# Kernel optimization log

Measured on AMD Instinct MI355X. Metric: run time of the kernel, lower is better.

The kernel has to match this reference:

```python
import jax, jax.numpy as jnp
import numpy as np

EMBED_DIM = 1024
NUM_HEADS = 16
HEAD_DIM = EMBED_DIM // NUM_HEADS
B, T = 4, 2048


def quantum_layer(x):
    # Exact closed form of the RY + CNOT-chain + PauliZ circuit:
    # expval(Z_i) = prod_{j<=i} cos(x_j)  (cumulative product along feature dim)
    return jnp.cumprod(jnp.cos(x), axis=-1)


def separate_heads(x):
    b, s, _ = x.shape
    return x.reshape(b, s, NUM_HEADS, HEAD_DIM).transpose(0, 2, 1, 3)  # (B,H,T,D)


def combine_heads(x):
    b, h, s, d = x.shape
    return x.transpose(0, 2, 1, 3).reshape(b, s, h * d)


def setup_inputs() -> dict:
    key = jax.random.key(0)
    ks = jax.random.split(key, 9)
    scale = 1.0 / np.sqrt(EMBED_DIM)
    return {
        "x": jax.random.normal(ks[0], (B, T, EMBED_DIM), dtype=jnp.float32),
        "Wq": jax.random.normal(ks[1], (EMBED_DIM, EMBED_DIM), dtype=jnp.float32) * scale,
        "bq": jax.random.normal(ks[2], (EMBED_DIM,), dtype=jnp.float32) * 0.01,
        "Wk": jax.random.normal(ks[3], (EMBED_DIM, EMBED_DIM), dtype=jnp.float32) * scale,
        "bk": jax.random.normal(ks[4], (EMBED_DIM,), dtype=jnp.float32) * 0.01,
        "Wv": jax.random.normal(ks[5], (EMBED_DIM, EMBED_DIM), dtype=jnp.float32) * scale,
        "bv": jax.random.normal(ks[6], (EMBED_DIM,), dtype=jnp.float32) * 0.01,
        "Wo": jax.random.normal(ks[7], (EMBED_DIM, EMBED_DIM), dtype=jnp.float32) * scale,
        "bo": jax.random.normal(ks[8], (EMBED_DIM,), dtype=jnp.float32) * 0.01,
    }


def reference(x, Wq, bq, Wk, bk, Wv, bv, Wo, bo):
    k = x @ Wk + bk
    q = x @ Wq + bq
    v = x @ Wv + bv
    # quantum circuit applied to q and k projections
    q = quantum_layer(q)
    k = quantum_layer(k)
    # NOTE: source swaps roles: kqv = (heads(k), heads(q), heads(v)); q, h, v = kqv
    qh = separate_heads(k)   # acts as query
    kh = separate_heads(q)   # acts as key
    vh = separate_heads(v)
    scores = jnp.einsum("bhqd,bhkd->bhqk", qh, kh) / jnp.sqrt(jnp.float32(HEAD_DIM))
    attn = jax.nn.softmax(scores, axis=-1)  # dropout is identity in eval
    out = jnp.einsum("bhqk,bhkd->bhqd", attn, vh)
    return combine_heads(out) @ Wo + bo
```

## Files before the change

### kernel.cpp

```cpp
#include <hip/hip_runtime.h>
#include <hip/hip_bf16.h>
#include <stdint.h>

#define B_ 4
#define T_ 2048
#define E_ 1024
#define H_ 16
#define D_ 64
#define M_ (B_ * T_)

typedef unsigned short u16;
typedef unsigned int u32;
typedef short s16x8 __attribute__((ext_vector_type(8)));
typedef unsigned short u16x8 __attribute__((ext_vector_type(8)));
typedef float f32x4 __attribute__((ext_vector_type(4)));
typedef unsigned int u32x2 __attribute__((ext_vector_type(2)));

#define LP_ 72

__device__ __forceinline__ u16 f2bf(float f) {
    __hip_bfloat16 h = __float2bfloat16(f);
    return __builtin_bit_cast(u16, h);
}
__device__ __forceinline__ float bf2f(u16 u) {
    unsigned int v = ((unsigned int)u) << 16;
    return __builtin_bit_cast(float, v);
}
__device__ __forceinline__ u32 pk2(float a, float b) {
    return (u32)f2bf(a) | ((u32)f2bf(b) << 16);
}

__device__ __forceinline__ int block_probe_is_bf16(const void* x, int tid) {
    const u16* p = (const u16*)x;
    u16 u = p[tid];
    int e = (u >> 7) & 0xFF;
    int ok = ((u & 0x7FFF) == 0 || (e >= 103 && e <= 133)) ? 1 : 0;
    return (__syncthreads_count(ok) >= 240) ? 1 : 0;
}

__device__ __forceinline__ void load_a_regs(
    int a_bf, const u16* abase_bf, const float* abase_f, int kk, u16x8 (&av)[4])
{
    if (a_bf) {
        #pragma unroll
        for (int j = 0; j < 4; j++) av[j] = *(const u16x8*)(abase_bf + kk + j * 8);
    } else {
        #pragma unroll
        for (int j = 0; j < 4; j++) {
            f32x4 t0 = *(const f32x4*)(abase_f + kk + j * 8);
            f32x4 t1 = *(const f32x4*)(abase_f + kk + j * 8 + 4);
            u16x8 o;
            #pragma unroll
            for (int e = 0; e < 4; e++) { o[e] = f2bf(t0[e]); o[4 + e] = f2bf(t1[e]); }
            av[j] = o;
        }
    }
}
__device__ __forceinline__ void load_b_regs(const u16* bbase, int kk, u16x8 (&bv)[4]) {
    #pragma unroll
    for (int j = 0; j < 4; j++) bv[j] = *(const u16x8*)(bbase + kk + j * 8);
}
__device__ __forceinline__ void write_lds72(
    u16* l, int srow, int soff, const u16x8 (&v)[4])
{
    #pragma unroll
    for (int j = 0; j < 4; j++)
        *(u16x8*)&l[srow * LP_ + soff + j * 8] = v[j];
}
__device__ __forceinline__ void mfma_tile72(
    const u16* al, const u16* bl, f32x4 (&acc)[4][4],
    int wm, int wn, int lane15, int quad)
{
    #pragma unroll
    for (int ks = 0; ks < 2; ks++) {
        s16x8 af[4], bfr[4];
        #pragma unroll
        for (int i = 0; i < 4; i++)
            af[i] = *(const s16x8*)&al[(wm + i * 16 + lane15) * LP_ + ks * 32 + quad * 8];
        #pragma unroll
        for (int j = 0; j < 4; j++)
            bfr[j] = *(const s16x8*)&bl[(wn + j * 16 + lane15) * LP_ + ks * 32 + quad * 8];
        #pragma unroll
        for (int i = 0; i < 4; i++)
            #pragma unroll
            for (int j = 0; j < 4; j++)
                acc[i][j] = __builtin_amdgcn_mfma_f32_16x16x32_bf16(af[i], bfr[j], acc[i][j], 0, 0, 0);
    }
}

__global__ __launch_bounds__(256) void transpose_w4_kernel(
    const void* __restrict__ w0, const void* __restrict__ w1,
    const void* __restrict__ w2, const void* __restrict__ w3,
    u16* __restrict__ o0, u16* __restrict__ o1,
    u16* __restrict__ o2, u16* __restrict__ o3,
    const void* __restrict__ xprobe)
{
    __shared__ u16 th[64][66];
    const int x = threadIdx.x, y = threadIdx.y;
    const int isbf = block_probe_is_bf16(xprobe, y * 64 + x);
    const int z = (int)blockIdx.z;
    const void* in = (z == 0) ? w0 : (z == 1) ? w1 : (z == 2) ? w2 : w3;
    u16* o = (z == 0) ? o0 : (z == 1) ? o1 : (z == 2) ? o2 : o3;
    const int r0 = blockIdx.y * 64;
    const int c0 = blockIdx.x * 64;
    #pragma unroll
    for (int j = 0; j < 16; j++) {
        const size_t idx = (size_t)(r0 + y * 16 + j) * E_ + c0 + x;
        float v = isbf ? bf2f(((const u16*)in)[idx]) : ((const float*)in)[idx];
        th[y * 16 + j][x] = f2bf(v);
    }
    __syncthreads();
    #pragma unroll
    for (int j = 0; j < 16; j++)
        o[(size_t)(c0 + y * 16 + j) * E_ + r0 + x] = th[x][y * 16 + j];
}

__global__ __launch_bounds__(256) void convert_bias_kernel(
    const void* __restrict__ bq, const void* __restrict__ bk,
    const void* __restrict__ bv, const void* __restrict__ bo,
    float* __restrict__ outb, const void* __restrict__ xprobe)
{
    const int isbf = block_probe_is_bf16(xprobe, threadIdx.x);
    const int i = blockIdx.x * 256 + threadIdx.x;
    const int w = blockIdx.y;
    const void* p = (w == 0) ? bq : (w == 1) ? bk : (w == 2) ? bv : bo;
    float v = isbf ? bf2f(((const u16*)p)[i]) : ((const float*)p)[i];
    outb[w * 1024 + i] = v;
}

__global__ __launch_bounds__(256) void gemm_f32out_kernel(
    const void* __restrict__ A, int a_mode, int m_base,
    const u16* __restrict__ Bt, const float* __restrict__ bias,
    float* __restrict__ Cout, int ldc)
{
    __shared__ u16 a_lds[128 * LP_];
    __shared__ u16 b_lds[128 * LP_];
    const int tid = threadIdx.x;
    const int isbf = block_probe_is_bf16(A, tid);
    const int a_bf = (a_mode < 0) ? isbf : a_mode;
    const int wave = tid >> 6, lane = tid & 63;
    const int lane15 = lane & 15, quad = lane >> 4;
    const int wm = (wave & 1) * 64, wn = (wave >> 1) * 64;
    const int nwg = (int)(gridDim.x * gridDim.y);
    const int lin = (int)(blockIdx.y * gridDim.x + blockIdx.x);
    const int swz = (lin & 7) * (nwg >> 3) + (lin >> 3);
    const int m0 = (swz / (int)gridDim.x) * 128;
    const int n0 = (swz % (int)gridDim.x) * 128;
    const int srow = tid >> 1;
    const int soff = (tid & 1) * 32;

    f32x4 acc[4][4];
    #pragma unroll
    for (int i = 0; i < 4; i++)
        #pragma unroll
        for (int j = 0; j < 4; j++) acc[i][j] = (f32x4)0.0f;

    const u16* abase_bf = (const u16*)A + (size_t)(m_base + m0 + srow) * E_ + soff;
    const float* abase_f = (const float*)A + (size_t)(m_base + m0 + srow) * E_ + soff;
    const u16* bbase = Bt + (size_t)(n0 + srow) * E_ + soff;

    u16x8 av[4], bv[4];
    load_a_regs(a_bf, abase_bf, abase_f, 0, av);
    load_b_regs(bbase, 0, bv);

    for (int kk = 0; kk < E_; kk += 64) {
        __syncthreads();
        write_lds72(a_lds, srow, soff, av);
        write_lds72(b_lds, srow, soff, bv);
        __syncthreads();
        if (kk + 64 < E_) {
            load_a_regs(a_bf, abase_bf, abase_f, kk + 64, av);
            load_b_regs(bbase, kk + 64, bv);
        }
        mfma_tile72(a_lds, b_lds, acc, wm, wn, lane15, quad);
    }

    #pragma unroll
    for (int j = 0; j < 4; j++) {
        const int col = n0 + wn + j * 16 + lane15;
        const float bb = bias[col];
        #pragma unroll
        for (int i = 0; i < 4; i++) {
            const int row = m0 + wm + i * 16 + quad * 4;
            #pragma unroll
            for (int r = 0; r < 4; r++)
                Cout[(size_t)(row + r) * ldc + col] = acc[i][j][r] + bb;
        }
    }
}

__global__ __launch_bounds__(256) void gemm_qkv_kernel(
    const void* __restrict__ A, const u16* __restrict__ Bt,
    const float* __restrict__ bias, float* __restrict__ Cout,
    u16* __restrict__ Vt)
{
    __shared__ u16 smem[2 * 128 * LP_];
    u16* a_lds = smem;
    u16* b_lds = smem + 128 * LP_;
    const int tid = threadIdx.x;
    const int isbf = block_probe_is_bf16(A, tid);
    const int wave = tid >> 6, lane = tid & 63;
    const int lane15 = lane & 15, quad = lane >> 4;
    const int wm = (wave & 1) * 64, wn = (wave >> 1) * 64;
    const int nwg = (int)(gridDim.x * gridDim.y);
    const int lin = (int)(blockIdx.y * gridDim.x + blockIdx.x);
    const int swz = (lin & 7) * (nwg >> 3) + (lin >> 3);
    const int m0 = (swz / (int)gridDim.x) * 128;
    const int n0 = (swz % (int)gridDim.x) * 128;
    const int srow = tid >> 1;
    const int soff = (tid & 1) * 32;

    f32x4 acc[4][4];
    #pragma unroll
    for (int i = 0; i < 4; i++)
        #pragma unroll
        for (int j = 0; j < 4; j++) acc[i][j] = (f32x4)0.0f;

    const u16* abase_bf = (const u16*)A + (size_t)(m0 + srow) * E_ + soff;
    const float* abase_f = (const float*)A + (size_t)(m0 + srow) * E_ + soff;
    const u16* bbase = Bt + (size_t)(n0 + srow) * E_ + soff;

    u16x8 av[4], bv[4];
    load_a_regs(isbf, abase_bf, abase_f, 0, av);
    load_b_regs(bbase, 0, bv);

    for (int kk = 0; kk < E_; kk += 64) {
        __syncthreads();
        write_lds72(a_lds, srow, soff, av);
        write_lds72(b_lds, srow, soff, bv);
        __syncthreads();
        if (kk + 64 < E_) {
            load_a_regs(isbf, abase_bf, abase_f, kk + 64, av);
            load_b_regs(bbase, kk + 64, bv);
        }
        mfma_tile72(a_lds, b_lds, acc, wm, wn, lane15, quad);
    }

    if (n0 < 2048) {
        #pragma unroll
        for (int j = 0; j < 4; j++) {
            const int col = n0 + wn + j * 16 + lane15;
            const float bb = bias[col];
            #pragma unroll
            for (int i = 0; i < 4; i++) {
                const int row = m0 + wm + i * 16 + quad * 4;
                #pragma unroll
                for (int r = 0; r < 4; r++)
                    Cout[(size_t)(row + r) * 2048 + col] = acc[i][j][r] + bb;
            }
        }
    } else {
        __syncthreads();
        u16* c_tile = smem;
        #pragma unroll
        for (int j = 0; j < 4; j++) {
            const float bb = bias[n0 + wn + j * 16 + lane15];
            #pragma unroll
            for (int i = 0; i < 4; i++)
                #pragma unroll
                for (int r = 0; r < 4; r++)
                    c_tile[(wm + i * 16 + quad * 4 + r) * 132 + wn + j * 16 + lane15] =
                        f2bf(acc[i][j][r] + bb);
        }
        __syncthreads();
        const int b = m0 >> 11, t0 = m0 & 2047;
        const int orow = tid >> 1, half = tid & 1;
        const int n0v = n0 - 2048;
        u16* dst = Vt + ((size_t)b * 1024 + n0v + orow) * T_ + t0 + half * 64;
        #pragma unroll
        for (int c = 0; c < 8; c++) {
            u16x8 o;
            #pragma unroll
            for (int e = 0; e < 8; e++)
                o[e] = c_tile[(half * 64 + c * 8 + e) * 132 + orow];
            *(u16x8*)(dst + c * 8) = o;
        }
    }
}

__global__ __launch_bounds__(256) void gemm_v_fused_kernel(
    const void* __restrict__ X, const u16* __restrict__ Bt,
    const float* __restrict__ bias, u16* __restrict__ Vt)
{
    __shared__ u16 smem[2 * 128 * 72];
    u16* a_lds = smem;
    u16* b_lds = smem + 128 * 72;
    const int tid = threadIdx.x;
    const int isbf = block_probe_is_bf16(X, tid);
    const int wave = tid >> 6, lane = tid & 63;
    const int lane15 = lane & 15, quad = lane >> 4;
    const int wm = (wave & 1) * 64, wn = (wave >> 1) * 64;
    const int nwg = (int)(gridDim.x * gridDim.y);
    const int lin = (int)(blockIdx.y * gridDim.x + blockIdx.x);
    const int swz = (lin & 7) * (nwg >> 3) + (lin >> 3);
    const int m0 = (swz / (int)gridDim.x) * 128;
    const int n0 = (swz % (int)gridDim.x) * 128;
    const int srow = tid >> 1;
    const int soff = (tid & 1) * 32;

    f32x4 acc[4][4];
    #pragma unroll
    for (int i = 0; i < 4; i++)
        #pragma unroll
        for (int j = 0; j < 4; j++) acc[i][j] = (f32x4)0.0f;

    const u16* abase_bf = (const u16*)X + (size_t)(m0 + srow) * E_ + soff;
    const float* abase_f = (const float*)X + (size_t)(m0 + srow) * E_ + soff;
    const u16* bbase = Bt + (size_t)(n0 + srow) * E_ + soff;

    u16x8 av[4], bv[4];
    load_a_regs(isbf, abase_bf, abase_f, 0, av);
    load_b_regs(bbase, 0, bv);

    for (int kk = 0; kk < E_; kk += 64) {
        __syncthreads();
        #pragma unroll
        for (int j = 0; j < 4; j++) {
            *(u16x8*)&a_lds[srow * 72 + soff + j * 8] = av[j];
            *(u16x8*)&b_lds[srow * 72 + soff + j * 8] = bv[j];
        }
        __syncthreads();
        if (kk + 64 < E_) {
            load_a_regs(isbf, abase_bf, abase_f, kk + 64, av);
            load_b_regs(bbase, kk + 64, bv);
        }
        #pragma unroll
        for (int ks = 0; ks < 2; ks++) {
            s16x8 af[4], bfr[4];
            #pragma unroll
            for (int i = 0; i < 4; i++)
                af[i] = *(const s16x8*)&a_lds[(wm + i * 16 + lane15) * 72 + ks * 32 + quad * 8];
            #pragma unroll
            for (int j = 0; j < 4; j++)
                bfr[j] = *(const s16x8*)&b_lds[(wn + j * 16 + lane15) * 72 + ks * 32 + quad * 8];
            #pragma unroll
            for (int i = 0; i < 4; i++)
                #pragma unroll
                for (int j = 0; j < 4; j++)
                    acc[i][j] = __builtin_amdgcn_mfma_f32_16x16x32_bf16(af[i], bfr[j], acc[i][j], 0, 0, 0);
        }
    }

    __syncthreads();
    u16* c_tile = smem;
    #pragma unroll
    for (int j = 0; j < 4; j++) {
        const float bb = bias[n0 + wn + j * 16 + lane15];
        #pragma unroll
        for (int i = 0; i < 4; i++)
            #pragma unroll
            for (int r = 0; r < 4; r++)
                c_tile[(wm + i * 16 + quad * 4 + r) * 132 + wn + j * 16 + lane15] =
                    f2bf(acc[i][j][r] + bb);
    }
    __syncthreads();
    const int b = m0 >> 11, t0 = m0 & 2047;
    const int orow = tid >> 1, half = tid & 1;
    u16* dst = Vt + ((size_t)b * 1024 + n0 + orow) * T_ + t0 + half * 64;
    #pragma unroll
    for (int c = 0; c < 8; c++) {
        u16x8 o;
        #pragma unroll
        for (int e = 0; e < 8; e++)
            o[e] = c_tile[(half * 64 + c * 8 + e) * 132 + orow];
        *(u16x8*)(dst + c * 8) = o;
    }
}

__global__ __launch_bounds__(256) void quantum2_kernel(
    const float* __restrict__ in, u16* __restrict__ key, u16* __restrict__ qry)
{
    const int wave = threadIdx.x >> 6, lane = threadIdx.x & 63;
    const int unit = (int)blockIdx.x * 4 + wave;
    const int row = unit >> 1, seg = unit & 1;
    const float* p = in + (size_t)row * 2048 + seg * 1024 + lane * 16;
    float v[16];
    #pragma unroll
    for (int j = 0; j < 16; j += 4) {
        f32x4 t = *(const f32x4*)(p + j);
        v[j] = t[0]; v[j + 1] = t[1]; v[j + 2] = t[2]; v[j + 3] = t[3];
    }
    float pl[16];
    float run = 1.0f;
    #pragma unroll
    for (int j = 0; j < 16; j++) { run *= cosf(v[j]); pl[j] = run; }
    float incl = run;
    #pragma unroll
    for (int off = 1; off < 64; off <<= 1) {
        float t = __shfl_up(incl, off);
        if (lane >= off) incl *= t;
    }
    float pref = __shfl_up(incl, 1);
    if (lane == 0) pref = 1.0f;
    u16x8 o0, o1;
    #pragma unroll
    for (int j = 0; j < 8; j++) {
        o0[j] = f2bf(pref * pl[j]);
        o1[j] = f2bf(pref * pl[j + 8]);
    }
    u16* outp = (seg ? qry : key) + (size_t)row * E_ + lane * 16;
    *(u16x8*)(outp) = o0;
    *(u16x8*)(outp + 8) = o1;
}

__global__ __launch_bounds__(256) void attn_kernel(
    const u16* __restrict__ Qrm, const u16* __restrict__ Krm,
    const u16* __restrict__ Vt, u16* __restrict__ Orm)
{
    __shared__ u16 k_lds[64 * 72];
    __shared__ u16 v_lds[64 * 72];
    __shared__ u16 p_lds[128 * 72];
    const int tid = threadIdx.x;
    const int wave = tid >> 6, lane = tid & 63;
    const int lane15 = lane & 15, quad = lane >> 4;

    const int lin = (int)(blockIdx.x + gridDim.x * blockIdx.y);
    const int swz = (lin & 7) * 128 + (lin >> 3);
    const int t0 = (swz & 15) * 128;
    const int bh = swz >> 4;
    const int b = bh >> 4, h = bh & 15;

    s16x8 qf[2][2];
    #pragma unroll
    for (int mt = 0; mt < 2; mt++)
        #pragma unroll
        for (int ks = 0; ks < 2; ks++) {
            const u16* src = Qrm
                + (size_t)(b * T_ + t0 + wave * 32 + mt * 16 + lane15) * E_
                + h * 64 + ks * 32 + quad * 8;
            u16x8 t = *(const u16x8*)src;
            u16x8 o;
            #pragma unroll
            for (int e = 0; e < 8; e++) o[e] = f2bf(bf2f(t[e]) * 0.125f);
            qf[mt][ks] = __builtin_bit_cast(s16x8, o);
        }

    f32x4 lsum4[2];
    f32x4 oacc[2][4];
    #pragma unroll
    for (int mt = 0; mt < 2; mt++) {
        lsum4[mt] = (f32x4)0.0f;
        #pragma unroll
        for (int n = 0; n < 4; n++) oacc[mt][n] = (f32x4)0.0f;
    }

    const u16* kbase = Krm + (size_t)(b * T_) * E_ + h * 64;
    const u16* vbase = Vt + (size_t)bh * 64 * T_;
    const int srow = tid >> 2;
    const int soff = (tid & 3) * 16;

    u16x8 kpre0, kpre1, vpre0, vpre1;
    {
        const u16* ksrc = kbase + (size_t)srow * E_ + soff;
        kpre0 = *(const u16x8*)(ksrc);
        kpre1 = *(const u16x8*)(ksrc + 8);
        const u16* vsrc = vbase + (size_t)srow * T_ + soff;
        vpre0 = *(const u16x8*)(vsrc);
        vpre1 = *(const u16x8*)(vsrc + 8);
    }

    for (int tk0 = 0; tk0 < T_; tk0 += 64) {
        __syncthreads();
        *(u16x8*)&k_lds[srow * 72 + soff]     = kpre0;
        *(u16x8*)&k_lds[srow * 72 + soff + 8] = kpre1;
        *(u16x8*)&v_lds[srow * 72 + soff]     = vpre0;
        *(u16x8*)&v_lds[srow * 72 + soff + 8] = vpre1;
        __syncthreads();

        if (tk0 + 64 < T_) {
            const u16* ksrc = kbase + (size_t)(tk0 + 64 + srow) * E_ + soff;
            kpre0 = *(const u16x8*)(ksrc);
            kpre1 = *(const u16x8*)(ksrc + 8);
            const u16* vsrc = vbase + (size_t)srow * T_ + tk0 + 64 + soff;
            vpre0 = *(const u16x8*)(vsrc);
            vpre1 = *(const u16x8*)(vsrc + 8);
        }

        f32x4 sacc[2][4];
        #pragma unroll
        for (int mt = 0; mt < 2; mt++)
            #pragma unroll
            for (int j = 0; j < 4; j++) sacc[mt][j] = (f32x4)0.0f;
        #pragma unroll
        for (int ks = 0; ks < 2; ks++) {
            s16x8 kb[4];
            #pragma unroll
            for (int j = 0; j < 4; j++)
                kb[j] = *(const s16x8*)&k_lds[(j * 16 + lane15) * 72 + ks * 32 + quad * 8];
            #pragma unroll
            for (int mt = 0; mt < 2; mt++)
                #pragma unroll
                for (int j = 0; j < 4; j++)
                    sacc[mt][j] = __builtin_amdgcn_mfma_f32_16x16x32_bf16(
                        kb[j], qf[mt][ks], sacc[mt][j], 0, 0, 0);
        }

        #pragma unroll
        for (int mt = 0; mt < 2; mt++)
            #pragma unroll
            for (int j = 0; j < 4; j++) {
                const f32x4 s = sacc[mt][j];
                const float p0 = __expf(s[0]);
                const float p1 = __expf(s[1]);
                const float p2 = __expf(s[2]);
                const float p3 = __expf(s[3]);
                lsum4[mt][0] += p0; lsum4[mt][1] += p1;
                lsum4[mt][2] += p2; lsum4[mt][3] += p3;
                u32x2 w;
                w[0] = pk2(p0, p1);
                w[1] = pk2(p2, p3);
                *(u32x2*)&p_lds[(wave * 32 + mt * 16 + lane15) * 72 + j * 16 + quad * 4] = w;
            }

        #pragma unroll
        for (int ks = 0; ks < 2; ks++) {
            s16x8 pa[2], vb[4];
            #pragma unroll
            for (int mt = 0; mt < 2; mt++)
                pa[mt] = *(const s16x8*)&p_lds[(wave * 32 + mt * 16 + lane15) * 72 + ks * 32 + quad * 8];
            #pragma unroll
            for (int n = 0; n < 4; n++)
                vb[n] = *(const s16x8*)&v_lds[(n * 16 + lane15) * 72 + ks * 32 + quad * 8];
            #pragma unroll
            for (int mt = 0; mt < 2; mt++)
                #pragma unroll
                for (int n = 0; n < 4; n++)
                    oacc[mt][n] = __builtin_amdgcn_mfma_f32_16x16x32_bf16(
                        pa[mt], vb[n], oacc[mt][n], 0, 0, 0);
        }
    }

    #pragma unroll
    for (int mt = 0; mt < 2; mt++) {
        float l = lsum4[mt][0] + lsum4[mt][1] + lsum4[mt][2] + lsum4[mt][3];
        l += __shfl_xor(l, 16);
        l += __shfl_xor(l, 32);
        #pragma unroll
        for (int r = 0; r < 4; r++) {
            const float lr = __shfl(l, quad * 4 + r);
            const float inv = 1.0f / lr;
            const size_t row = (size_t)(b * T_ + t0 + wave * 32 + mt * 16 + quad * 4 + r);
            #pragma unroll
            for (int n = 0; n < 4; n++)
                Orm[row * E_ + h * 64 + n * 16 + lane15] = f2bf(oacc[mt][n][r] * inv);
        }
    }
}

extern "C" void kernel_launch(void* const* d_in, const int* in_sizes, int n_in,
                              void* d_out, int out_size, void* d_ws, size_t ws_size,
                              hipStream_t stream) {
    (void)in_sizes; (void)n_in; (void)out_size;
    const void* x  = d_in[0];
    const void* Wq = d_in[1];
    const void* bq = d_in[2];
    const void* Wk = d_in[3];
    const void* bk = d_in[4];
    const void* Wv = d_in[5];
    const void* bv = d_in[6];
    const void* Wo = d_in[7];
    const void* bo = d_in[8];

    char* ws = (char*)d_ws;
    const size_t MB = 1024 * 1024;
    u16*   wt_o   = (u16*)(ws);
    float* biasf  = (float*)(ws + 2 * MB);
    u16*   wt_qkv = (u16*)(ws + 3 * MB);
    u16*   key    = (u16*)(ws + 9 * MB);
    u16*   qry    = (u16*)(ws + 25 * MB);

    transpose_w4_kernel<<<dim3(16, 16, 4), dim3(64, 4), 0, stream>>>(
        Wq, Wk, Wv, Wo,
        wt_qkv, wt_qkv + 1024 * 1024, wt_qkv + 2 * 1024 * 1024, wt_o, x);
    convert_bias_kernel<<<dim3(4, 4), 256, 0, stream>>>(
        bq, bk, bv, bo, biasf, x);

    if (ws_size >= (size_t)121 * MB) {
        u16*   vt  = (u16*)(ws + 41 * MB);
        float* tmp = (float*)(ws + 57 * MB);
        u16*   orm = (u16*)(ws + 57 * MB);
        gemm_qkv_kernel<<<dim3(24, 64), 256, 0, stream>>>(
            x, wt_qkv, biasf, tmp, vt);
        quantum2_kernel<<<4096, 256, 0, stream>>>(tmp, key, qry);
        attn_kernel<<<dim3(16, 64), 256, 0, stream>>>(qry, key, vt, orm);
        gemm_f32out_kernel<<<dim3(8, 64), 256, 0, stream>>>(
            orm, 1, 0, wt_o, biasf + 3 * 1024, (float*)d_out, 1024);
    } else {
        float* tmp = (float*)(ws + 41 * MB);
        u16*   vt  = (u16*)(ws + 41 * MB);
        u16*   orm = (u16*)(ws + 57 * MB);
        for (int hh = 0; hh < 2; hh++) {
            gemm_f32out_kernel<<<dim3(16, 32), 256, 0, stream>>>(
                x, -1, hh * 4096, wt_qkv, biasf, tmp, 2048);
            quantum2_kernel<<<2048, 256, 0, stream>>>(
                tmp, key + (size_t)hh * 4096 * E_, qry + (size_t)hh * 4096 * E_);
        }
        gemm_v_fused_kernel<<<dim3(8, 64), 256, 0, stream>>>(
            x, wt_qkv + 2 * 1024 * 1024, biasf + 2 * 1024, vt);
        attn_kernel<<<dim3(16, 64), 256, 0, stream>>>(qry, key, vt, orm);
        gemm_f32out_kernel<<<dim3(8, 64), 256, 0, stream>>>(
            orm, 1, 0, wt_o, biasf + 3 * 1024, (float*)d_out, 1024);
    }
}
```

Baseline: 376.2 us.

## Stage QKV GEMM tiles via global_load_lds with double-buffered LDS pipeline

Rewrites the QKV projection GEMM main loop to copy bf16 A and B tiles directly from global memory into LDS using the global_load_lds builtin. The tiles are double-buffered so the next K-slice loads while MFMAs run on the current one, with explicit vmcnt waits and raw barriers. This removes the register round-trip and the separate LDS writes. In exchange LDS use doubles, the unpadded 64-wide layout may cause bank conflicts, and the fp32 fallback path still converts through registers. The MFMA section is also wrapped in s_setprio.

Measured after the change: 410.6 us. +9.2%, slower.

```diff
diff --git a/kernel.cpp b/kernel.cpp
--- a/kernel.cpp
+++ b/kernel.cpp
@@ -30,6 +30,15 @@
     return (u32)f2bf(a) | ((u32)f2bf(b) << 16);
 }
 
+typedef __attribute__((address_space(1))) const void as1_void;
+typedef __attribute__((address_space(3))) void as3_void;
+__device__ __forceinline__ void gload16(const void* g, void* l) {
+    __builtin_amdgcn_global_load_lds(
+        reinterpret_cast<as1_void*>(reinterpret_cast<uintptr_t>(g)),
+        reinterpret_cast<as3_void*>(reinterpret_cast<uintptr_t>(l)),
+        16, 0, 0);
+}
+
 __device__ __forceinline__ int block_probe_is_bf16(const void* x, int tid) {
     const u16* p = (const u16*)x;
     u16 u = p[tid];
@@ -80,6 +89,45 @@
         #pragma unroll
         for (int j = 0; j < 4; j++)
             bfr[j] = *(const s16x8*)&bl[(wn + j * 16 + lane15) * LP_ + ks * 32 + quad * 8];
+        #pragma unroll
+        for (int i = 0; i < 4; i++)
+            #pragma unroll
+            for (int j = 0; j < 4; j++)
+                acc[i][j] = __builtin_amdgcn_mfma_f32_16x16x32_bf16(af[i], bfr[j], acc[i][j], 0, 0, 0);
+    }
+}
+
+__device__ __forceinline__ void stage_bf64(const u16* g, int kk, u16* l, int wave) {
+    #pragma unroll
+    for (int j = 0; j < 4; j++)
+        gload16(g + (size_t)j * 8 * E_ + kk, l + (wave * 4 + j) * 512);
+}
+__device__ __forceinline__ void stage_a_f32_64(
+    const float* abase_f, int kk, u16* al, int srow, int soff)
+{
+    #pragma unroll
+    for (int j = 0; j < 4; j++) {
+        f32x4 t0 = *(const f32x4*)(abase_f + kk + j * 8);
+        f32x4 t1 = *(const f32x4*)(abase_f + kk + j * 8 + 4);
+        u16x8 o;
+        #pragma unroll
+        for (int e = 0; e < 4; e++) { o[e] = f2bf(t0[e]); o[4 + e] = f2bf(t1[e]); }
+        *(u16x8*)&al[srow * 64 + soff + j * 8] = o;
+    }
+}
+__device__ __forceinline__ void mfma_tile64(
+    const u16* al, const u16* bl, f32x4 (&acc)[4][4],
+    int wm, int wn, int lane15, int quad)
+{
+    #pragma unroll
+    for (int ks = 0; ks < 2; ks++) {
+        s16x8 af[4], bfr[4];
+        #pragma unroll
+        for (int i = 0; i < 4; i++)
+            af[i] = *(const s16x8*)&al[(wm + i * 16 + lane15) * 64 + ks * 32 + quad * 8];
+        #pragma unroll
+        for (int j = 0; j < 4; j++)
+            bfr[j] = *(const s16x8*)&bl[(wn + j * 16 + lane15) * 64 + ks * 32 + quad * 8];
         #pragma unroll
         for (int i = 0; i < 4; i++)
             #pragma unroll
@@ -194,9 +242,7 @@
     const float* __restrict__ bias, float* __restrict__ Cout,
     u16* __restrict__ Vt)
 {
-    __shared__ u16 smem[2 * 128 * LP_];
-    u16* a_lds = smem;
-    u16* b_lds = smem + 128 * LP_;
+    __shared__ u16 smem[4 * 128 * 64];
     const int tid = threadIdx.x;
     const int isbf = block_probe_is_bf16(A, tid);
     const int wave = tid >> 6, lane = tid & 63;
@@ -207,33 +253,54 @@
     const int swz = (lin & 7) * (nwg >> 3) + (lin >> 3);
     const int m0 = (swz / (int)gridDim.x) * 128;
     const int n0 = (swz % (int)gridDim.x) * 128;
+
+    f32x4 acc[4][4];
+    #pragma unroll
+    for (int i = 0; i < 4; i++)
+        #pragma unroll
+        for (int j = 0; j < 4; j++) acc[i][j] = (f32x4)0.0f;
+
+    const int g_r = wave * 32 + (lane >> 3);
+    const int g_c = (lane & 7) * 8;
+    const u16* ga = (const u16*)A + (size_t)(m0 + g_r) * E_ + g_c;
+    const u16* gb = Bt + (size_t)(n0 + g_r) * E_ + g_c;
     const int srow = tid >> 1;
     const int soff = (tid & 1) * 32;
-
-    f32x4 acc[4][4];
-    #pragma unroll
-    for (int i = 0; i < 4; i++)
-        #pragma unroll
-        for (int j = 0; j < 4; j++) acc[i][j] = (f32x4)0.0f;
-
-    const u16* abase_bf = (const u16*)A + (size_t)(m0 + srow) * E_ + soff;
     const float* abase_f = (const float*)A + (size_t)(m0 + srow) * E_ + soff;
-    const u16* bbase = Bt + (size_t)(n0 + srow) * E_ + soff;
-
-    u16x8 av[4], bv[4];
-    load_a_regs(isbf, abase_bf, abase_f, 0, av);
-    load_b_regs(bbase, 0, bv);
-
-    for (int kk = 0; kk < E_; kk += 64) {
-        __syncthreads();
-        write_lds72(a_lds, srow, soff, av);
-        write_lds72(b_lds, srow, soff, bv);
-        __syncthreads();
-        if (kk + 64 < E_) {
-            load_a_regs(isbf, abase_bf, abase_f, kk + 64, av);
-            load_b_regs(bbase, kk + 64, bv);
-        }
-        mfma_tile72(a_lds, b_lds, acc, wm, wn, lane15, quad);
+
+    if (isbf) stage_bf64(ga, 0, smem, wave);
+    else      stage_a_f32_64(abase_f, 0, smem, srow, soff);
+    stage_bf64(gb, 0, smem + 2 * 8192, wave);
+
+    #pragma unroll
+    for (int t = 0; t < 16; ++t) {
+        const int cur = t & 1;
+        if (t < 15) {
+            const int nxt = cur ^ 1;
+            if (isbf) stage_bf64(ga, (t + 1) * 64, smem + nxt * 8192, wave);
+            else      stage_a_f32_64(abase_f, (t + 1) * 64, smem + nxt * 8192, srow, soff);
+            stage_bf64(gb, (t + 1) * 64, smem + (2 + nxt) * 8192, wave);
+        }
+        if (isbf) {
+            if (t < 15) asm volatile("s_waitcnt vmcnt(8)" ::: "memory");
+            else        asm volatile("s_waitcnt vmcnt(0)" ::: "memory");
+            __builtin_amdgcn_sched_barrier(0);
+            __builtin_amdgcn_s_barrier();
+            __builtin_amdgcn_sched_barrier(0);
+        } else {
+            __syncthreads();
+        }
+        __builtin_amdgcn_s_setprio(1);
+        mfma_tile64(smem + cur * 8192, smem + (2 + cur) * 8192,
+                    acc, wm, wn, lane15, quad);
+        __builtin_amdgcn_s_setprio(0);
+        if (isbf) {
+            __builtin_amdgcn_sched_barrier(0);
+            __builtin_amdgcn_s_barrier();
+            __builtin_amdgcn_sched_barrier(0);
+        } else {
+            __syncthreads();
+        }
     }
 
     if (n0 < 2048) {
```
